# Optimization experiments

Measured on AMD Instinct MI355X. Metric: run time of the kernel, lower is better.

The kernel has to match this reference:

```python
import jax, jax.numpy as jnp
import numpy as np

L = 65536
D = 256

def setup_inputs() -> dict:
    key = jax.random.key(0)
    k1, k2, k3 = jax.random.split(key, 3)
    K = jax.random.normal(k1, (L, D), dtype=jnp.float32)
    V = jax.random.normal(k2, (L, D), dtype=jnp.float32)
    q = jax.random.normal(k3, (D,), dtype=jnp.float32)  # nn.Parameter(torch.randn(d_model))
    return {"K": K, "V": V, "q": q, "mode": 0}

def reference(K, V, q, mode):
    # s[i] = <K[i], q>; online-softmax recurrence over the sequence dim.
    s = K @ q  # [L]
    neg_inf = jnp.float32(-jnp.inf)

    def step(carry, inp):
        m_prev, u_prev, w_prev = carry
        s_i, v_i = inp
        m = jnp.maximum(m_prev, s_i)
        e_prev = jnp.exp(m_prev - m)
        e_curr = jnp.exp(s_i - m)
        u = u_prev * e_prev + e_curr
        w = w_prev * e_prev + v_i * e_curr  # [D]
        return (m, u, w), w / u

    init = (neg_inf, jnp.float32(0.0), jnp.zeros((D,), dtype=V.dtype))
    _, out = jax.lax.scan(step, init, (s, V))  # out: [L, D]
    return out
```

## Files before the change

### kernel.cpp

```cpp
#include <hip/hip_runtime.h>
#include <math.h>

#define L_TOTAL 65536
#define D_DIM   256
#define C_ROWS  32
#define N_CHUNK (L_TOTAL / C_ROWS)
#define SUPER   32
#define N_SUPER (N_CHUNK / SUPER)

typedef float vf4 __attribute__((ext_vector_type(4)));

__global__ __launch_bounds__(256) void kA_aggregate(
    const float* __restrict__ K, const float* __restrict__ V,
    const float* __restrict__ q,
    float* __restrict__ s_g, float* __restrict__ cm,
    float* __restrict__ cu, float* __restrict__ cw)
{
    const int t = threadIdx.x;
    const int c = blockIdx.x;
    const int r0 = c * C_ROWS;
    const int wave = t >> 6, lane = t & 63;

    __shared__ float s_lds[C_ROWS];
    __shared__ vf4  pw_lds[4][64];

    vf4 v4[8];
    const vf4* Vp = reinterpret_cast<const vf4*>(V + (size_t)(r0 + wave * 8) * D_DIM) + lane;
    #pragma unroll
    for (int k = 0; k < 8; ++k) v4[k] = Vp[(size_t)k * (D_DIM / 4)];

    const vf4 q4 = *reinterpret_cast<const vf4*>(q + 4 * lane);
    const vf4* Kp = reinterpret_cast<const vf4*>(K + (size_t)(r0 + wave * 8) * D_DIM) + lane;
    #pragma unroll
    for (int k = 0; k < 8; ++k) {
        const vf4 kv = __builtin_nontemporal_load(Kp + (size_t)k * (D_DIM / 4));
        float d = kv.x * q4.x + kv.y * q4.y + kv.z * q4.z + kv.w * q4.w;
        #pragma unroll
        for (int off = 32; off > 0; off >>= 1) d += __shfl_xor(d, off, 64);
        if (lane == 0) s_lds[wave * 8 + k] = d;
    }
    __syncthreads();

    if (t < C_ROWS) s_g[r0 + t] = s_lds[t];

    float m_c = -INFINITY;
    #pragma unroll
    for (int j = 0; j < C_ROWS; ++j) m_c = fmaxf(m_c, s_lds[j]);
    float u_c = 0.f;
    #pragma unroll
    for (int j = 0; j < C_ROWS; ++j) u_c += __expf(s_lds[j] - m_c);

    vf4 pw = {0.f, 0.f, 0.f, 0.f};
    #pragma unroll
    for (int k = 0; k < 8; ++k) {
        const float cf = __expf(s_lds[wave * 8 + k] - m_c);
        pw = pw + cf * v4[k];
    }
    pw_lds[wave][lane] = pw;
    __syncthreads();

    if (t < 64) {
        const vf4 w4 = (pw_lds[0][t] + pw_lds[1][t]) + (pw_lds[2][t] + pw_lds[3][t]);
        reinterpret_cast<vf4*>(cw + (size_t)c * D_DIM)[t] = w4;
    }
    if (t == 0) { cm[c] = m_c; cu[c] = u_c; }
}

__global__ __launch_bounds__(256) void kCB_scan(
    const float* __restrict__ cm, const float* __restrict__ cu,
    const float* __restrict__ cw,
    float* __restrict__ pm, float* __restrict__ pu,
    float* __restrict__ gsup,
    float* __restrict__ pwl, float* __restrict__ T)
{
    const int t = threadIdx.x;
    const int S = blockIdx.x;
    __shared__ float Lm[256], Lu[256];
    __shared__ float pmL[N_CHUNK + 1];
    __shared__ float ca[SUPER], cb[SUPER];

    float am[8], au[8];
    float M = -INFINITY, U = 0.f;
    #pragma unroll
    for (int j = 0; j < 8; ++j) {
        am[j] = cm[8 * t + j]; au[j] = cu[8 * t + j];
        const float mm = fmaxf(M, am[j]);
        U = U * __expf(M - mm) + au[j] * __expf(am[j] - mm);
        M = mm;
    }
    Lm[t] = M; Lu[t] = U;
    float Mi = M, Ui = U;
    __syncthreads();
    for (int off = 1; off < 256; off <<= 1) {
        float m1 = 0.f, u1 = 0.f;
        const bool act = (t >= off);
        if (act) { m1 = Lm[t - off]; u1 = Lu[t - off]; }
        __syncthreads();
        if (act) {
            const float mm = fmaxf(m1, Mi);
            Ui = u1 * __expf(m1 - mm) + Ui * __expf(Mi - mm);
            Mi = mm;
            Lm[t] = Mi; Lu[t] = Ui;
        }
        __syncthreads();
    }
    float Me = (t == 0) ? -INFINITY : Lm[t - 1];
    float Ue = (t == 0) ? 0.f : Lu[t - 1];
    #pragma unroll
    for (int j = 0; j < 8; ++j) {
        pmL[8 * t + j] = Me;
        if (S == 0) { pm[8 * t + j] = Me; pu[8 * t + j] = Ue; }
        const float mm = fmaxf(Me, am[j]);
        Ue = Ue * __expf(Me - mm) + au[j] * __expf(am[j] - mm);
        Me = mm;
    }
    if (t == 255) {
        pmL[N_CHUNK] = Me;
        if (S == 0) { pm[N_CHUNK] = Me; pu[N_CHUNK] = Ue; }
    }
    __syncthreads();

    float wv[SUPER];
    const float* cwp = cw + (size_t)S * SUPER * D_DIM + t;
    #pragma unroll
    for (int j = 0; j < SUPER; ++j) wv[j] = cwp[(size_t)j * D_DIM];

    if (t < SUPER) {
        const int c = S * SUPER + t;
        ca[t] = __expf(pmL[c] - pmL[c + 1]);
        cb[t] = __expf(cm[c] - pmL[c + 1]);
    }
    if (t == 0)
        gsup[S] = __expf(pmL[S * SUPER] - pmL[S * SUPER + SUPER]);
    __syncthreads();

    float PW = 0.f;
    float* pwlp = pwl + (size_t)S * SUPER * D_DIM + t;
    #pragma unroll
    for (int j = 0; j < SUPER; ++j) {
        pwlp[(size_t)j * D_DIM] = PW;
        PW = PW * ca[j] + wv[j] * cb[j];
    }
    T[(size_t)S * D_DIM + t] = PW;
}

__global__ __launch_bounds__(256) void kF_output(
    const float* __restrict__ V, const float* __restrict__ s_g,
    const float* __restrict__ pm, const float* __restrict__ pu,
    const float* __restrict__ pwl, const float* __restrict__ T,
    const float* __restrict__ gsup,
    float* __restrict__ out)
{
    const int t = threadIdx.x;
    const int c = blockIdx.x;
    const int S = c / SUPER;
    const int r0 = c * C_ROWS;
    const int wave = t >> 6, lane = t & 63;

    __shared__ float sa[C_ROWS], se[C_ROWS], sri[C_ROWS];
    __shared__ vf4 seedL[64];
    __shared__ vf4 seg[4][64];
    __shared__ float asL[4];

    vf4 v4[8];
    const vf4* Vp = reinterpret_cast<const vf4*>(V + (size_t)(r0 + wave * 8) * D_DIM) + lane;
    #pragma unroll
    for (int k = 0; k < 8; ++k) v4[k] = Vp[(size_t)k * (D_DIM / 4)];

    if (wave == 0) {
        const float pmc = pm[c];
        const float puc = pu[c];
        float s_val = -INFINITY;
        if (lane < C_ROWS) s_val = s_g[r0 + lane];
        float m = s_val, u = 1.0f;
        #pragma unroll
        for (int off = 1; off < C_ROWS; off <<= 1) {
            const float m1 = __shfl_up(m, off, 32);
            const float u1 = __shfl_up(u, off, 32);
            if ((lane & 31) >= off) {
                const float mm = fmaxf(m1, m);
                u = u1 * __expf(m1 - mm) + u * __expf(m - mm);
                m = mm;
            }
        }
        const float m_row = fmaxf(pmc, m);
        const float u_row = puc * __expf(pmc - m_row) + u * __expf(m - m_row);
        const float m_prev_raw = __shfl_up(m_row, 1, 32);
        const float m_prev = ((lane & 31) == 0) ? pmc : m_prev_raw;
        if (lane < C_ROWS) {
            sa[lane]  = __expf(m_prev - m_row);
            se[lane]  = __expf(s_val - m_row);
            sri[lane] = 1.0f / u_row;
        }
    } else if (wave == 1) {
        const float pmc = pm[c];
        const float pmS = pm[S * SUPER];
        vf4 SW = {0.f, 0.f, 0.f, 0.f};
        const vf4* T4 = reinterpret_cast<const vf4*>(T) + lane;
        #pragma unroll 8
        for (int Sp = 0; Sp < S; ++Sp) {
            const float g = gsup[Sp];
            SW = SW * g + T4[(size_t)Sp * (D_DIM / 4)];
        }
        const float gf = (c == 0) ? 0.f : __expf(pmS - pmc);
        const vf4 sp = reinterpret_cast<const vf4*>(pwl + (size_t)c * D_DIM)[lane];
        seedL[lane] = SW * gf + sp;
    }
    __syncthreads();

    vf4 B = {0.f, 0.f, 0.f, 0.f};
    float A = 1.f;
    #pragma unroll
    for (int k = 0; k < 8; ++k) {
        const int j = wave * 8 + k;
        B = B * sa[j] + v4[k] * se[j];
        A *= sa[j];
    }
    seg[wave][lane] = B;
    if (lane == 0) asL[wave] = A;
    __syncthreads();

    vf4 W = seedL[lane];
    for (int p = 0; p < wave; ++p)
        W = W * asL[p] + seg[p][lane];

    float* Op = out + (size_t)(r0 + wave * 8) * D_DIM + 4 * lane;
    #pragma unroll
    for (int k = 0; k < 8; ++k) {
        const int j = wave * 8 + k;
        W = W * sa[j] + v4[k] * se[j];
        __builtin_nontemporal_store(W * sri[j],
                                    reinterpret_cast<vf4*>(Op + (size_t)k * D_DIM));
    }
}

extern "C" void kernel_launch(void* const* d_in, const int* in_sizes, int n_in,
                              void* d_out, int out_size, void* d_ws, size_t ws_size,
                              hipStream_t stream) {
    const float* K = (const float*)d_in[0];
    const float* V = (const float*)d_in[1];
    const float* q = (const float*)d_in[2];
    float* out = (float*)d_out;

    float* ws   = (float*)d_ws;
    float* s_g  = ws;
    float* cm   = s_g + L_TOTAL;
    float* cu   = cm + N_CHUNK;
    float* pm   = cu + N_CHUNK;
    float* pu   = pm + (N_CHUNK + 16);
    float* gsup = pu + (N_CHUNK + 16);
    float* cw   = gsup + 128;
    float* pwl  = cw + (size_t)N_CHUNK * D_DIM;
    float* T    = pwl + (size_t)N_CHUNK * D_DIM;

    kA_aggregate<<<N_CHUNK, 256, 0, stream>>>(K, V, q, s_g, cm, cu, cw);
    kCB_scan<<<N_SUPER, 256, 0, stream>>>(cm, cu, cw, pm, pu, gsup, pwl, T);
    kF_output<<<N_CHUNK, 256, 0, stream>>>(V, s_g, pm, pu, pwl, T, gsup, out);
}
```

Baseline: 185.3 us.

## Fuse three-pass chunked scan into one cooperative kernel with grid syncs

Replaces the aggregate/scan/output launches with a single cooperative kernel of 1024 blocks, each covering 64 rows. V stays in registers across two grid-wide barriers, so V is read once instead of twice and the s and per-chunk prefix arrays no longer round-trip through global memory. Every block redundantly recomputes the block-level max/sum scan in LDS, and the first 32 blocks build the super-block totals. The old three-kernel path remains as a fallback if the cooperative launch fails. The trade-offs are grid-sync cost, a residency requirement of 4 blocks per CU with high register use (16 vf4 of V per thread), and serial seed loops of up to 31 and 31 steps in wave 1.

```diff
diff --git a/kernel.cpp b/kernel.cpp
--- a/kernel.cpp
+++ b/kernel.cpp
@@ -1,14 +1,209 @@
 #include <hip/hip_runtime.h>
+#include <hip/hip_cooperative_groups.h>
 #include <math.h>
+
+namespace cg = cooperative_groups;
 
 #define L_TOTAL 65536
 #define D_DIM   256
+
+typedef float vf4 __attribute__((ext_vector_type(4)));
+
+#define NB    1024
+#define RB    64
+#define NSUP  32
+#define SBLK  32
+
+__global__ __launch_bounds__(256, 4) void kFused(
+    const float* __restrict__ K, const float* __restrict__ V,
+    const float* __restrict__ q,
+    float* __restrict__ cm, float* __restrict__ cu,
+    float* __restrict__ cw, float* __restrict__ T,
+    float* __restrict__ out)
+{
+    const int t = threadIdx.x;
+    const int b = blockIdx.x;
+    const int S = b >> 5;
+    const int jloc = b & 31;
+    const int r0 = b * RB;
+    const int wave = t >> 6, lane = t & 63;
+
+    __shared__ float s_lds[RB];
+    __shared__ vf4  wbuf[4][64];
+    __shared__ float Lm[256], Lu[256];
+    __shared__ float pmL[NB + 1], puL[NB + 1];
+    __shared__ float sa[RB], se[RB], sri[RB];
+    __shared__ vf4  seedL[64];
+    __shared__ float asL[4];
+
+    vf4 v4[16];
+    {
+        const vf4* Vp = reinterpret_cast<const vf4*>(V + (size_t)(r0 + wave * 16) * D_DIM) + lane;
+        #pragma unroll
+        for (int k = 0; k < 16; ++k) v4[k] = Vp[(size_t)k * (D_DIM / 4)];
+
+        const vf4 q4 = *reinterpret_cast<const vf4*>(q + 4 * lane);
+        const vf4* Kp = reinterpret_cast<const vf4*>(K + (size_t)(r0 + wave * 16) * D_DIM) + lane;
+        #pragma unroll
+        for (int k = 0; k < 16; ++k) {
+            const vf4 kv = __builtin_nontemporal_load(Kp + (size_t)k * (D_DIM / 4));
+            float d = kv.x * q4.x + kv.y * q4.y + kv.z * q4.z + kv.w * q4.w;
+            #pragma unroll
+            for (int off = 32; off > 0; off >>= 1) d += __shfl_xor(d, off, 64);
+            if (lane == 0) s_lds[wave * 16 + k] = d;
+        }
+    }
+    __syncthreads();
+
+    float m_b = -INFINITY;
+    #pragma unroll
+    for (int j = 0; j < RB; ++j) m_b = fmaxf(m_b, s_lds[j]);
+    float u_b = 0.f;
+    #pragma unroll
+    for (int j = 0; j < RB; ++j) u_b += __expf(s_lds[j] - m_b);
+
+    {
+        vf4 pw = {0.f, 0.f, 0.f, 0.f};
+        #pragma unroll
+        for (int k = 0; k < 16; ++k)
+            pw = pw + __expf(s_lds[wave * 16 + k] - m_b) * v4[k];
+        wbuf[wave][lane] = pw;
+    }
+    __syncthreads();
+    if (t < 64) {
+        const vf4 w4 = (wbuf[0][t] + wbuf[1][t]) + (wbuf[2][t] + wbuf[3][t]);
+        reinterpret_cast<vf4*>(cw)[(size_t)b * 64 + t] = w4;
+    }
+    if (t == 0) { cm[b] = m_b; cu[b] = u_b; }
+
+    __threadfence();
+    cg::this_grid().sync();
+
+    float am[4], au[4];
+    float M = -INFINITY, U = 0.f;
+    #pragma unroll
+    for (int j = 0; j < 4; ++j) {
+        am[j] = cm[4 * t + j]; au[j] = cu[4 * t + j];
+        const float mm = fmaxf(M, am[j]);
+        U = U * __expf(M - mm) + au[j] * __expf(am[j] - mm);
+        M = mm;
+    }
+    Lm[t] = M; Lu[t] = U;
+    float Mi = M, Ui = U;
+    __syncthreads();
+    for (int off = 1; off < 256; off <<= 1) {
+        float m1 = 0.f, u1 = 0.f;
+        const bool act = (t >= off);
+        if (act) { m1 = Lm[t - off]; u1 = Lu[t - off]; }
+        __syncthreads();
+        if (act) {
+            const float mm = fmaxf(m1, Mi);
+            Ui = u1 * __expf(m1 - mm) + Ui * __expf(Mi - mm);
+            Mi = mm;
+            Lm[t] = Mi; Lu[t] = Ui;
+        }
+        __syncthreads();
+    }
+    float Me = (t == 0) ? -INFINITY : Lm[t - 1];
+    float Ue = (t == 0) ? 0.f : Lu[t - 1];
+    #pragma unroll
+    for (int j = 0; j < 4; ++j) {
+        pmL[4 * t + j] = Me; puL[4 * t + j] = Ue;
+        const float mm = fmaxf(Me, am[j]);
+        Ue = Ue * __expf(Me - mm) + au[j] * __expf(am[j] - mm);
+        Me = mm;
+    }
+    if (t == 255) { pmL[NB] = Me; puL[NB] = Ue; }
+    __syncthreads();
+
+    if (b < NSUP && t < 64) {
+        vf4 PW = {0.f, 0.f, 0.f, 0.f};
+        const vf4* cw4 = reinterpret_cast<const vf4*>(cw);
+        #pragma unroll 8
+        for (int j = 0; j < SBLK; ++j) {
+            const int bb = b * SBLK + j;
+            const float caj = __expf(pmL[bb] - pmL[bb + 1]);
+            const float cbj = __expf(cm[bb] - pmL[bb + 1]);
+            PW = PW * caj + cw4[(size_t)bb * 64 + t] * cbj;
+        }
+        reinterpret_cast<vf4*>(T)[(size_t)b * 64 + t] = PW;
+    }
+    __threadfence();
+    cg::this_grid().sync();
+
+    if (wave == 0) {
+        const float pmc = pmL[b], puc = puL[b];
+        const float s_val = s_lds[lane];
+        float m = s_val, u = 1.0f;
+        #pragma unroll
+        for (int off = 1; off < 64; off <<= 1) {
+            const float m1 = __shfl_up(m, off, 64);
+            const float u1 = __shfl_up(u, off, 64);
+            if (lane >= off) {
+                const float mm = fmaxf(m1, m);
+                u = u1 * __expf(m1 - mm) + u * __expf(m - mm);
+                m = mm;
+            }
+        }
+        const float m_row = fmaxf(pmc, m);
+        const float u_row = puc * __expf(pmc - m_row) + u * __expf(m - m_row);
+        const float mpr = __shfl_up(m_row, 1, 64);
+        const float m_prev = (lane == 0) ? pmc : mpr;
+        sa[lane]  = __expf(m_prev - m_row);
+        se[lane]  = __expf(s_val - m_row);
+        sri[lane] = 1.0f / u_row;
+    } else if (wave == 1) {
+        const float pmc = pmL[b];
+        const float pmS = pmL[S * SBLK];
+        const vf4* cw4 = reinterpret_cast<const vf4*>(cw);
+        vf4 PW = {0.f, 0.f, 0.f, 0.f};
+        for (int j = 0; j < jloc; ++j) {
+            const int bb = S * SBLK + j;
+            const float caj = __expf(pmL[bb] - pmL[bb + 1]);
+            const float cbj = __expf(cm[bb] - pmL[bb + 1]);
+            PW = PW * caj + cw4[(size_t)bb * 64 + lane] * cbj;
+        }
+        const vf4* T4 = reinterpret_cast<const vf4*>(T);
+        vf4 SW = {0.f, 0.f, 0.f, 0.f};
+        for (int Sp = 0; Sp < S; ++Sp) {
+            const float g = __expf(pmL[Sp * SBLK] - pmL[Sp * SBLK + SBLK]);
+            SW = SW * g + T4[(size_t)Sp * 64 + lane];
+        }
+        const float gf = (b == 0) ? 0.f : __expf(pmS - pmc);
+        seedL[lane] = SW * gf + PW;
+    }
+    __syncthreads();
+
+    vf4 B = {0.f, 0.f, 0.f, 0.f};
+    float A = 1.f;
+    #pragma unroll
+    for (int k = 0; k < 16; ++k) {
+        const int j = wave * 16 + k;
+        B = B * sa[j] + v4[k] * se[j];
+        A *= sa[j];
+    }
+    wbuf[wave][lane] = B;
+    if (lane == 0) asL[wave] = A;
+    __syncthreads();
+
+    vf4 W = seedL[lane];
+    for (int p = 0; p < wave; ++p)
+        W = W * asL[p] + wbuf[p][lane];
+
+    float* Op = out + (size_t)(r0 + wave * 16) * D_DIM + 4 * lane;
+    #pragma unroll
+    for (int k = 0; k < 16; ++k) {
+        const int j = wave * 16 + k;
+        W = W * sa[j] + v4[k] * se[j];
+        __builtin_nontemporal_store(W * sri[j],
+                                    reinterpret_cast<vf4*>(Op + (size_t)k * D_DIM));
+    }
+}
+
 #define C_ROWS  32
 #define N_CHUNK (L_TOTAL / C_ROWS)
 #define SUPER   32
 #define N_SUPER (N_CHUNK / SUPER)
-
-typedef float vf4 __attribute__((ext_vector_type(4)));
 
 __global__ __launch_bounds__(256) void kA_aggregate(
     const float* __restrict__ K, const float* __restrict__ V,
@@ -52,10 +247,8 @@
 
     vf4 pw = {0.f, 0.f, 0.f, 0.f};
     #pragma unroll
-    for (int k = 0; k < 8; ++k) {
-        const float cf = __expf(s_lds[wave * 8 + k] - m_c);
-        pw = pw + cf * v4[k];
-    }
+    for (int k = 0; k < 8; ++k)
+        pw = pw + __expf(s_lds[wave * 8 + k] - m_c) * v4[k];
     pw_lds[wave][lane] = pw;
     __syncthreads();
 
@@ -241,19 +434,37 @@
     const float* V = (const float*)d_in[1];
     const float* q = (const float*)d_in[2];
     float* out = (float*)d_out;
-
-    float* ws   = (float*)d_ws;
-    float* s_g  = ws;
-    float* cm   = s_g + L_TOTAL;
-    float* cu   = cm + N_CHUNK;
-    float* pm   = cu + N_CHUNK;
-    float* pu   = pm + (N_CHUNK + 16);
-    float* gsup = pu + (N_CHUNK + 16);
-    float* cw   = gsup + 128;
-    float* pwl  = cw + (size_t)N_CHUNK * D_DIM;
-    float* T    = pwl + (size_t)N_CHUNK * D_DIM;
-
-    kA_aggregate<<<N_CHUNK, 256, 0, stream>>>(K, V, q, s_g, cm, cu, cw);
-    kCB_scan<<<N_SUPER, 256, 0, stream>>>(cm, cu, cw, pm, pu, gsup, pwl, T);
-    kF_output<<<N_CHUNK, 256, 0, stream>>>(V, s_g, pm, pu, pwl, T, gsup, out);
+    float* ws = (float*)d_ws;
+
+    float* cmF = ws;
+    float* cuF = cmF + NB;
+    float* TF  = cuF + NB;
+    float* cwF = TF + (size_t)NSUP * D_DIM;
+    float* fb  = cwF + (size_t)NB * D_DIM;
+
+    void* kargs[8];
+    kargs[0] = (void*)&K;  kargs[1] = (void*)&V;   kargs[2] = (void*)&q;
+    kargs[3] = (void*)&cmF; kargs[4] = (void*)&cuF; kargs[5] = (void*)&cwF;
+    kargs[6] = (void*)&TF;  kargs[7] = (void*)&out;
+
+    hipError_t err = hipLaunchCooperativeKernel(
+        reinterpret_cast<const void*>(&kFused),
+        dim3(NB), dim3(256), kargs, 0, stream);
+
+    if (err != hipSuccess) {
+        (void)hipGetLastError();
+        float* s_g  = fb;
+        float* cm   = s_g + L_TOTAL;
+        float* cu   = cm + N_CHUNK;
+        float* pm   = cu + N_CHUNK;
+        float* pu   = pm + (N_CHUNK + 16);
+        float* gsup = pu + (N_CHUNK + 16);
+        float* cw   = gsup + 128;
+        float* pwl  = cw + (size_t)N_CHUNK * D_DIM;
+        float* T    = pwl + (size_t)N_CHUNK * D_DIM;
+
+        kA_aggregate<<<N_CHUNK, 256, 0, stream>>>(K, V, q, s_g, cm, cu, cw);
+        kCB_scan<<<N_SUPER, 256, 0, stream>>>(cm, cu, cw, pm, pu, gsup, pwl, T);
+        kF_output<<<N_CHUNK, 256, 0, stream>>>(V, s_g, pm, pu, pwl, T, gsup, out);
+    }
 }
```

After: 559.0 us. 202% more time.

## Replace three-kernel scan with single-pass decoupled look-back scan

Applied to the files above, without the earlier changes.

Merges the aggregate, scan and output kernels into one single-pass kernel that uses decoupled look-back. Each 64-row block publishes its aggregate and its inclusive prefix through flags and spins on predecessor flags to build its seed. V is now read only once and the second read, the intermediate workspace traffic and the extra launches go away. In exchange it depends on blocks being scheduled in order and on spin-waiting, which can serialize blocks or stall if the dispatch order does not hold.

```diff
diff --git a/kernel.cpp b/kernel.cpp
--- a/kernel.cpp
+++ b/kernel.cpp
@@ -3,231 +3,198 @@
 
 #define L_TOTAL 65536
 #define D_DIM   256
-#define C_ROWS  32
-#define N_CHUNK (L_TOTAL / C_ROWS)
-#define SUPER   32
-#define N_SUPER (N_CHUNK / SUPER)
+#define RB      64
+#define NB      (L_TOTAL / RB)
 
 typedef float vf4 __attribute__((ext_vector_type(4)));
 
-__global__ __launch_bounds__(256) void kA_aggregate(
+__global__ __launch_bounds__(256) void kClear(int* __restrict__ flag)
+{
+    const int i = blockIdx.x * 256 + threadIdx.x;
+    if (i < NB) flag[i] = 0;
+}
+
+__global__ __launch_bounds__(256) void kScan(
     const float* __restrict__ K, const float* __restrict__ V,
     const float* __restrict__ q,
-    float* __restrict__ s_g, float* __restrict__ cm,
-    float* __restrict__ cu, float* __restrict__ cw)
-{
-    const int t = threadIdx.x;
-    const int c = blockIdx.x;
-    const int r0 = c * C_ROWS;
-    const int wave = t >> 6, lane = t & 63;
-
-    __shared__ float s_lds[C_ROWS];
-    __shared__ vf4  pw_lds[4][64];
-
-    vf4 v4[8];
-    const vf4* Vp = reinterpret_cast<const vf4*>(V + (size_t)(r0 + wave * 8) * D_DIM) + lane;
-    #pragma unroll
-    for (int k = 0; k < 8; ++k) v4[k] = Vp[(size_t)k * (D_DIM / 4)];
-
-    const vf4 q4 = *reinterpret_cast<const vf4*>(q + 4 * lane);
-    const vf4* Kp = reinterpret_cast<const vf4*>(K + (size_t)(r0 + wave * 8) * D_DIM) + lane;
-    #pragma unroll
-    for (int k = 0; k < 8; ++k) {
-        const vf4 kv = __builtin_nontemporal_load(Kp + (size_t)k * (D_DIM / 4));
-        float d = kv.x * q4.x + kv.y * q4.y + kv.z * q4.z + kv.w * q4.w;
-        #pragma unroll
-        for (int off = 32; off > 0; off >>= 1) d += __shfl_xor(d, off, 64);
-        if (lane == 0) s_lds[wave * 8 + k] = d;
-    }
-    __syncthreads();
-
-    if (t < C_ROWS) s_g[r0 + t] = s_lds[t];
-
-    float m_c = -INFINITY;
-    #pragma unroll
-    for (int j = 0; j < C_ROWS; ++j) m_c = fmaxf(m_c, s_lds[j]);
-    float u_c = 0.f;
-    #pragma unroll
-    for (int j = 0; j < C_ROWS; ++j) u_c += __expf(s_lds[j] - m_c);
-
-    vf4 pw = {0.f, 0.f, 0.f, 0.f};
-    #pragma unroll
-    for (int k = 0; k < 8; ++k) {
-        const float cf = __expf(s_lds[wave * 8 + k] - m_c);
-        pw = pw + cf * v4[k];
-    }
-    pw_lds[wave][lane] = pw;
-    __syncthreads();
-
-    if (t < 64) {
-        const vf4 w4 = (pw_lds[0][t] + pw_lds[1][t]) + (pw_lds[2][t] + pw_lds[3][t]);
-        reinterpret_cast<vf4*>(cw + (size_t)c * D_DIM)[t] = w4;
-    }
-    if (t == 0) { cm[c] = m_c; cu[c] = u_c; }
-}
-
-__global__ __launch_bounds__(256) void kCB_scan(
-    const float* __restrict__ cm, const float* __restrict__ cu,
-    const float* __restrict__ cw,
-    float* __restrict__ pm, float* __restrict__ pu,
-    float* __restrict__ gsup,
-    float* __restrict__ pwl, float* __restrict__ T)
-{
-    const int t = threadIdx.x;
-    const int S = blockIdx.x;
-    __shared__ float Lm[256], Lu[256];
-    __shared__ float pmL[N_CHUNK + 1];
-    __shared__ float ca[SUPER], cb[SUPER];
-
-    float am[8], au[8];
-    float M = -INFINITY, U = 0.f;
-    #pragma unroll
-    for (int j = 0; j < 8; ++j) {
-        am[j] = cm[8 * t + j]; au[j] = cu[8 * t + j];
-        const float mm = fmaxf(M, am[j]);
-        U = U * __expf(M - mm) + au[j] * __expf(am[j] - mm);
-        M = mm;
-    }
-    Lm[t] = M; Lu[t] = U;
-    float Mi = M, Ui = U;
-    __syncthreads();
-    for (int off = 1; off < 256; off <<= 1) {
-        float m1 = 0.f, u1 = 0.f;
-        const bool act = (t >= off);
-        if (act) { m1 = Lm[t - off]; u1 = Lu[t - off]; }
-        __syncthreads();
-        if (act) {
-            const float mm = fmaxf(m1, Mi);
-            Ui = u1 * __expf(m1 - mm) + Ui * __expf(Mi - mm);
-            Mi = mm;
-            Lm[t] = Mi; Lu[t] = Ui;
-        }
-        __syncthreads();
-    }
-    float Me = (t == 0) ? -INFINITY : Lm[t - 1];
-    float Ue = (t == 0) ? 0.f : Lu[t - 1];
-    #pragma unroll
-    for (int j = 0; j < 8; ++j) {
-        pmL[8 * t + j] = Me;
-        if (S == 0) { pm[8 * t + j] = Me; pu[8 * t + j] = Ue; }
-        const float mm = fmaxf(Me, am[j]);
-        Ue = Ue * __expf(Me - mm) + au[j] * __expf(am[j] - mm);
-        Me = mm;
-    }
-    if (t == 255) {
-        pmL[N_CHUNK] = Me;
-        if (S == 0) { pm[N_CHUNK] = Me; pu[N_CHUNK] = Ue; }
-    }
-    __syncthreads();
-
-    float wv[SUPER];
-    const float* cwp = cw + (size_t)S * SUPER * D_DIM + t;
-    #pragma unroll
-    for (int j = 0; j < SUPER; ++j) wv[j] = cwp[(size_t)j * D_DIM];
-
-    if (t < SUPER) {
-        const int c = S * SUPER + t;
-        ca[t] = __expf(pmL[c] - pmL[c + 1]);
-        cb[t] = __expf(cm[c] - pmL[c + 1]);
-    }
-    if (t == 0)
-        gsup[S] = __expf(pmL[S * SUPER] - pmL[S * SUPER + SUPER]);
-    __syncthreads();
-
-    float PW = 0.f;
-    float* pwlp = pwl + (size_t)S * SUPER * D_DIM + t;
-    #pragma unroll
-    for (int j = 0; j < SUPER; ++j) {
-        pwlp[(size_t)j * D_DIM] = PW;
-        PW = PW * ca[j] + wv[j] * cb[j];
-    }
-    T[(size_t)S * D_DIM + t] = PW;
-}
-
-__global__ __launch_bounds__(256) void kF_output(
-    const float* __restrict__ V, const float* __restrict__ s_g,
-    const float* __restrict__ pm, const float* __restrict__ pu,
-    const float* __restrict__ pwl, const float* __restrict__ T,
-    const float* __restrict__ gsup,
+    float* __restrict__ ma, float* __restrict__ ua,
+    float* __restrict__ mi, float* __restrict__ ui,
+    float* __restrict__ wa, float* __restrict__ wi,
+    int* __restrict__ flag,
     float* __restrict__ out)
 {
     const int t = threadIdx.x;
-    const int c = blockIdx.x;
-    const int S = c / SUPER;
-    const int r0 = c * C_ROWS;
+    const int b = blockIdx.x;
+    const int r0 = b * RB;
     const int wave = t >> 6, lane = t & 63;
 
-    __shared__ float sa[C_ROWS], se[C_ROWS], sri[C_ROWS];
-    __shared__ vf4 seedL[64];
-    __shared__ vf4 seg[4][64];
+    __shared__ float s_lds[RB];
+    __shared__ vf4  wbuf[4][64];
+    __shared__ vf4  wlocL[64];
+    __shared__ vf4  seedL[64];
+    __shared__ float mwin[NB], uwin[NB];
+    __shared__ float mloc[RB], uloc[RB];
+    __shared__ float sa[RB], se[RB], sri[RB];
     __shared__ float asL[4];
-
-    vf4 v4[8];
-    const vf4* Vp = reinterpret_cast<const vf4*>(V + (size_t)(r0 + wave * 8) * D_DIM) + lane;
-    #pragma unroll
-    for (int k = 0; k < 8; ++k) v4[k] = Vp[(size_t)k * (D_DIM / 4)];
-
-    if (wave == 0) {
-        const float pmc = pm[c];
-        const float puc = pu[c];
-        float s_val = -INFINITY;
-        if (lane < C_ROWS) s_val = s_g[r0 + lane];
-        float m = s_val, u = 1.0f;
-        #pragma unroll
-        for (int off = 1; off < C_ROWS; off <<= 1) {
-            const float m1 = __shfl_up(m, off, 32);
-            const float u1 = __shfl_up(u, off, 32);
-            if ((lane & 31) >= off) {
+    __shared__ float pmS, puS;
+    __shared__ int   nS, liS;
+
+    vf4 v4[16];
+    {
+        const vf4* Vp = reinterpret_cast<const vf4*>(V + (size_t)(r0 + wave * 16) * D_DIM) + lane;
+        #pragma unroll
+        for (int k = 0; k < 16; ++k) v4[k] = Vp[(size_t)k * (D_DIM / 4)];
+
+        const vf4 q4 = *reinterpret_cast<const vf4*>(q + 4 * lane);
+        const vf4* Kp = reinterpret_cast<const vf4*>(K + (size_t)(r0 + wave * 16) * D_DIM) + lane;
+        #pragma unroll
+        for (int k = 0; k < 16; ++k) {
+            const vf4 kv = __builtin_nontemporal_load(Kp + (size_t)k * (D_DIM / 4));
+            float d = kv.x * q4.x + kv.y * q4.y + kv.z * q4.z + kv.w * q4.w;
+            #pragma unroll
+            for (int off = 32; off > 0; off >>= 1) d += __shfl_xor(d, off, 64);
+            if (lane == 0) s_lds[wave * 16 + k] = d;
+        }
+    }
+    __syncthreads();
+
+    float m_b = -INFINITY;
+    #pragma unroll
+    for (int j = 0; j < RB; ++j) m_b = fmaxf(m_b, s_lds[j]);
+    float u_b = 0.f;
+    #pragma unroll
+    for (int j = 0; j < RB; ++j) u_b += __expf(s_lds[j] - m_b);
+    {
+        vf4 pw = {0.f, 0.f, 0.f, 0.f};
+        #pragma unroll
+        for (int k = 0; k < 16; ++k)
+            pw = pw + __expf(s_lds[wave * 16 + k] - m_b) * v4[k];
+        wbuf[wave][lane] = pw;
+    }
+    __syncthreads();
+    if (t < 64) {
+        const vf4 w4 = (wbuf[0][t] + wbuf[1][t]) + (wbuf[2][t] + wbuf[3][t]);
+        wlocL[t] = w4;
+        reinterpret_cast<vf4*>(wa + (size_t)b * D_DIM)[t] = w4;
+        if (t == 0) { ma[b] = m_b; ua[b] = u_b; }
+    }
+    __syncthreads();
+    if (t == 0)
+        __hip_atomic_store(&flag[b], 1, __ATOMIC_RELEASE, __HIP_MEMORY_SCOPE_AGENT);
+
+    if (wave == 1) {
+        const float sv = s_lds[lane];
+        float m = sv, u = 1.f;
+        #pragma unroll
+        for (int off = 1; off < 64; off <<= 1) {
+            const float m1 = __shfl_up(m, off, 64);
+            const float u1 = __shfl_up(u, off, 64);
+            if (lane >= off) {
                 const float mm = fmaxf(m1, m);
                 u = u1 * __expf(m1 - mm) + u * __expf(m - mm);
                 m = mm;
             }
         }
-        const float m_row = fmaxf(pmc, m);
-        const float u_row = puc * __expf(pmc - m_row) + u * __expf(m - m_row);
-        const float m_prev_raw = __shfl_up(m_row, 1, 32);
-        const float m_prev = ((lane & 31) == 0) ? pmc : m_prev_raw;
-        if (lane < C_ROWS) {
-            sa[lane]  = __expf(m_prev - m_row);
-            se[lane]  = __expf(s_val - m_row);
-            sri[lane] = 1.0f / u_row;
-        }
-    } else if (wave == 1) {
-        const float pmc = pm[c];
-        const float pmS = pm[S * SUPER];
-        vf4 SW = {0.f, 0.f, 0.f, 0.f};
-        const vf4* T4 = reinterpret_cast<const vf4*>(T) + lane;
-        #pragma unroll 8
-        for (int Sp = 0; Sp < S; ++Sp) {
-            const float g = gsup[Sp];
-            SW = SW * g + T4[(size_t)Sp * (D_DIM / 4)];
-        }
-        const float gf = (c == 0) ? 0.f : __expf(pmS - pmc);
-        const vf4 sp = reinterpret_cast<const vf4*>(pwl + (size_t)c * D_DIM)[lane];
-        seedL[lane] = SW * gf + sp;
-    }
-    __syncthreads();
+        mloc[lane] = m; uloc[lane] = u;
+    }
+
+    if (wave == 0) {
+        int n = 0, li = 0;
+        if (b > 0) {
+            int base = b - 1;
+            while (true) {
+                const int p = base - lane;
+                int f;
+                while (true) {
+                    f = (p < 0) ? 2
+                        : __hip_atomic_load(&flag[p], __ATOMIC_RELAXED, __HIP_MEMORY_SCOPE_AGENT);
+                    if (__all(f != 0)) break;
+                    __builtin_amdgcn_s_sleep(8);
+                }
+                (void)__hip_atomic_load(&flag[b - 1], __ATOMIC_ACQUIRE, __HIP_MEMORY_SCOPE_AGENT);
+                const unsigned long long m2 = __ballot(f == 2);
+                const int l2 = (m2 == 0) ? 64 : (__ffsll((long long)m2) - 1);
+                float mv = -INFINITY, uv = 0.f;
+                if (lane < l2)                 { mv = ma[p]; uv = ua[p]; }
+                else if (lane == l2 && p >= 0) { mv = mi[p]; uv = ui[p]; }
+                const int inc = (l2 < 64 && (base - l2) >= 0) ? 1 : 0;
+                const int cnt = (l2 < 64) ? (l2 + inc) : 64;
+                if (lane < cnt) { mwin[n + lane] = mv; uwin[n + lane] = uv; }
+                n += cnt;
+                if (l2 < 64) { li = inc; break; }
+                base -= 64;
+            }
+        }
+        float mp = -INFINITY;
+        for (int i = lane; i < n; i += 64) mp = fmaxf(mp, mwin[i]);
+        #pragma unroll
+        for (int off = 32; off > 0; off >>= 1) mp = fmaxf(mp, __shfl_xor(mp, off, 64));
+        float up = 0.f;
+        for (int i = lane; i < n; i += 64) {
+            const float bt = __expf(mwin[i] - mp);
+            mwin[i] = bt;
+            up += bt * uwin[i];
+        }
+        #pragma unroll
+        for (int off = 32; off > 0; off >>= 1) up += __shfl_xor(up, off, 64);
+        if (lane == 0) { pmS = mp; puS = up; nS = n; liS = li; }
+    }
+    __syncthreads();
+
+    {
+        const int n = nS, li = liS;
+        vf4 acc = {0.f, 0.f, 0.f, 0.f};
+        for (int i = wave; i < n; i += 4) {
+            const int p = b - 1 - i;
+            const float bt = mwin[i];
+            const float* basep = (li && i == n - 1) ? wi : wa;
+            acc = acc + bt * reinterpret_cast<const vf4*>(basep + (size_t)p * D_DIM)[lane];
+        }
+        wbuf[wave][lane] = acc;
+    }
+    __syncthreads();
+
+    if (t < 64) {
+        const vf4 pW = (wbuf[0][t] + wbuf[1][t]) + (wbuf[2][t] + wbuf[3][t]);
+        seedL[t] = pW;
+        const float pm = pmS, pu = puS;
+        const float m_inc = fmaxf(pm, m_b);
+        const float b1 = __expf(pm - m_inc), b2 = __expf(m_b - m_inc);
+        reinterpret_cast<vf4*>(wi + (size_t)b * D_DIM)[t] = pW * b1 + wlocL[t] * b2;
+        if (t == 0) { mi[b] = m_inc; ui[b] = pu * b1 + u_b * b2; }
+
+        const float ml = mloc[t], ul = uloc[t];
+        const float m_row = fmaxf(pm, ml);
+        const float u_row = pu * __expf(pm - m_row) + ul * __expf(ml - m_row);
+        const float mprev = (t == 0) ? pm : fmaxf(pm, mloc[t - 1]);
+        sa[t]  = __expf(mprev - m_row);
+        se[t]  = __expf(s_lds[t] - m_row);
+        sri[t] = 1.f / u_row;
+    }
+    __syncthreads();
+    if (t == 0)
+        __hip_atomic_store(&flag[b], 2, __ATOMIC_RELEASE, __HIP_MEMORY_SCOPE_AGENT);
 
     vf4 B = {0.f, 0.f, 0.f, 0.f};
     float A = 1.f;
     #pragma unroll
-    for (int k = 0; k < 8; ++k) {
-        const int j = wave * 8 + k;
+    for (int k = 0; k < 16; ++k) {
+        const int j = wave * 16 + k;
         B = B * sa[j] + v4[k] * se[j];
         A *= sa[j];
     }
-    seg[wave][lane] = B;
+    wbuf[wave][lane] = B;
     if (lane == 0) asL[wave] = A;
     __syncthreads();
 
     vf4 W = seedL[lane];
     for (int p = 0; p < wave; ++p)
-        W = W * asL[p] + seg[p][lane];
-
-    float* Op = out + (size_t)(r0 + wave * 8) * D_DIM + 4 * lane;
-    #pragma unroll
-    for (int k = 0; k < 8; ++k) {
-        const int j = wave * 8 + k;
+        W = W * asL[p] + wbuf[p][lane];
+
+    float* Op = out + (size_t)(r0 + wave * 16) * D_DIM + 4 * lane;
+    #pragma unroll
+    for (int k = 0; k < 16; ++k) {
+        const int j = wave * 16 + k;
         W = W * sa[j] + v4[k] * se[j];
         __builtin_nontemporal_store(W * sri[j],
                                     reinterpret_cast<vf4*>(Op + (size_t)k * D_DIM));
@@ -242,18 +209,15 @@
     const float* q = (const float*)d_in[2];
     float* out = (float*)d_out;
 
-    float* ws   = (float*)d_ws;
-    float* s_g  = ws;
-    float* cm   = s_g + L_TOTAL;
-    float* cu   = cm + N_CHUNK;
-    float* pm   = cu + N_CHUNK;
-    float* pu   = pm + (N_CHUNK + 16);
-    float* gsup = pu + (N_CHUNK + 16);
-    float* cw   = gsup + 128;
-    float* pwl  = cw + (size_t)N_CHUNK * D_DIM;
-    float* T    = pwl + (size_t)N_CHUNK * D_DIM;
-
-    kA_aggregate<<<N_CHUNK, 256, 0, stream>>>(K, V, q, s_g, cm, cu, cw);
-    kCB_scan<<<N_SUPER, 256, 0, stream>>>(cm, cu, cw, pm, pu, gsup, pwl, T);
-    kF_output<<<N_CHUNK, 256, 0, stream>>>(V, s_g, pm, pu, pwl, T, gsup, out);
+    float* ws  = (float*)d_ws;
+    int*   flag = (int*)ws;
+    float* ma  = ws + 1024;
+    float* ua  = ma + NB;
+    float* mi  = ua + NB;
+    float* ui  = mi + NB;
+    float* wa  = ui + NB;
+    float* wi  = wa + (size_t)NB * D_DIM;
+
+    kClear<<<(NB + 255) / 256, 256, 0, stream>>>(flag);
+    kScan<<<NB, 256, 0, stream>>>(K, V, q, ma, ua, mi, ui, wa, wi, flag, out);
 }
```

Result: slower. 298.0 us (+60.9%).
